# Performance work log

Hardware: AMD Instinct MI355X
Metric: run time of the kernel (lower is better)

The kernel has to match this reference:

```python
import jax, jax.numpy as jnp
import numpy as np

P = 2048
D = 1024
H = 16
DH = D // H
HID = 32


def setup_inputs() -> dict:
    key = jax.random.key(0)
    ks = jax.random.split(key, 10)
    s = 0.02
    return {
        "x": jax.random.normal(ks[0], (P, D), jnp.float32),
        "rel": jax.random.normal(ks[1], (P, P, 2), jnp.float32),
        "w_qkv": jax.random.normal(ks[2], (D, 3 * D), jnp.float32) * s,
        "w_proj": jax.random.normal(ks[3], (D, D), jnp.float32) * s,
        "rpb_w1": jax.random.normal(ks[4], (2, HID), jnp.float32) * s,
        "rpb_b1": jnp.zeros((HID,), jnp.float32),
        "rpb_w2": jax.random.normal(ks[5], (HID, HID), jnp.float32) * s,
        "rpb_b2": jnp.zeros((HID,), jnp.float32),
        "rpb_w3": jax.random.normal(ks[6], (HID, 1), jnp.float32) * s,
        "rpb_b3": jnp.zeros((1,), jnp.float32),
    }


def reference(x, rel, w_qkv, w_proj, rpb_w1, rpb_b1, rpb_w2, rpb_b2, rpb_w3, rpb_b3):
    scale = 1.0 / np.sqrt(DH)
    qkv = x @ w_qkv                                   # [P, 3D]
    q, k, v = jnp.split(qkv, 3, axis=-1)
    # [P, D] -> [H, P, DH]
    q = q.reshape(P, H, DH).transpose(1, 0, 2)
    k = k.reshape(P, H, DH).transpose(1, 0, 2)
    v = v.reshape(P, H, DH).transpose(1, 0, 2)
    logits = jnp.einsum('hpd,hqd->hpq', q, k) * scale  # [H, P, P]
    # RelPosBias MLP: (dx,dy) -> scalar, applied over [P, P, 2]
    hcur = jax.nn.relu(rel @ rpb_w1 + rpb_b1)
    hcur = jax.nn.relu(hcur @ rpb_w2 + rpb_b2)
    bias = (hcur @ rpb_w3 + rpb_b3)[..., 0]            # [P, P]
    logits = logits + bias[None]
    attn = jax.nn.softmax(logits, axis=-1)
    out = jnp.einsum('hpq,hqd->hpd', attn, v)          # [H, P, DH]
    out = out.transpose(1, 0, 2).reshape(P, D)
    return out @ w_proj
```

## Files before the change

kernel.cpp:

```cpp
#include <hip/hip_runtime.h>
#include <hip/hip_bf16.h>
#include <type_traits>

typedef __attribute__((ext_vector_type(8))) short bf16x8;
typedef __attribute__((ext_vector_type(4))) float floatx4;
typedef __attribute__((ext_vector_type(2))) float float2v;

__device__ __forceinline__ float bf2f(unsigned short u) {
    union { unsigned int x; float f; } v; v.x = ((unsigned int)u) << 16; return v.f;
}
__device__ __forceinline__ unsigned short f2bf(float f) {
    union { float f; unsigned int u; } v; v.f = f;
    unsigned int x = v.u;
    unsigned int r = x + 0x7fffu + ((x >> 16) & 1u);
    return (unsigned short)(r >> 16);
}

typedef const __attribute__((address_space(1))) unsigned int u32_g;
typedef __attribute__((address_space(3))) unsigned int u32_l;
__device__ __forceinline__ void gld_lds16(const void* g, void* l) {
    __builtin_amdgcn_global_load_lds((u32_g*)g, (u32_l*)l, 16, 0, 0);
}

__device__ __forceinline__ void trans32(const float* __restrict__ in,
                                        unsigned short* __restrict__ out,
                                        int K, int N, int bx, int by,
                                        unsigned short (*T)[33]) {
    const int n0 = bx * 32, k0 = by * 32;
    const int r = threadIdx.x >> 3;
    const int c4 = (threadIdx.x & 7) * 4;
    float4 v = *reinterpret_cast<const float4*>(in + (size_t)(k0 + r) * N + n0 + c4);
    T[c4 + 0][r] = f2bf(v.x);
    T[c4 + 1][r] = f2bf(v.y);
    T[c4 + 2][r] = f2bf(v.z);
    T[c4 + 3][r] = f2bf(v.w);
    __syncthreads();
    ushort4 o = {T[r][c4], T[r][c4 + 1], T[r][c4 + 2], T[r][c4 + 3]};
    *reinterpret_cast<ushort4*>(out + (size_t)(n0 + r) * K + k0 + c4) = o;
}

__global__ __launch_bounds__(256) void prep(const float* __restrict__ x,
                                            unsigned short* __restrict__ xb,
                                            const float* __restrict__ wq,
                                            unsigned short* __restrict__ wqT,
                                            const float* __restrict__ wp,
                                            unsigned short* __restrict__ wpT) {
    __shared__ unsigned short T[32][33];
    const int b = blockIdx.x;
    if (b < 1024) {
        size_t i = ((size_t)b * 256 + threadIdx.x) * 8;
        float4 a = *reinterpret_cast<const float4*>(x + i);
        float4 c = *reinterpret_cast<const float4*>(x + i + 4);
        unsigned short t[8] = {f2bf(a.x), f2bf(a.y), f2bf(a.z), f2bf(a.w),
                               f2bf(c.x), f2bf(c.y), f2bf(c.z), f2bf(c.w)};
        *reinterpret_cast<uint4*>(xb + i) = *reinterpret_cast<const uint4*>(t);
    } else if (b < 4096) {
        int t = b - 1024;
        trans32(wq, wqT, 1024, 3072, t % 96, t / 96, T);
    } else {
        int t = b - 4096;
        trans32(wp, wpT, 1024, 1024, t % 32, t / 32, T);
    }
}

template<int BN, typename TC>
__global__ __launch_bounds__(256) void gemm_abt(const unsigned short* __restrict__ A,
                                                const unsigned short* __restrict__ Bt,
                                                TC* __restrict__ C,
                                                int M, int N, int K) {
    constexpr int NT = BN / 32;
    __shared__ __align__(16) unsigned short As[64 * 32];
    __shared__ __align__(16) unsigned short Bs[BN * 32];

    const int tid = threadIdx.x;
    const int wave = tid >> 6;
    const int lane = tid & 63;
    const int m15 = lane & 15;
    const int quad = lane >> 4;
    const int wm = wave >> 1;
    const int wn = wave & 1;
    const int m0 = blockIdx.y * 64;
    const int n0 = blockIdx.x * BN;

    const int srow = lane >> 2;
    const int scol = (lane & 3) * 8;

    floatx4 acc[2][NT];
#pragma unroll
    for (int mt = 0; mt < 2; mt++)
#pragma unroll
        for (int nt = 0; nt < NT; nt++) acc[mt][nt] = {0.f, 0.f, 0.f, 0.f};

    for (int k0 = 0; k0 < K; k0 += 32) {
        gld_lds16(A + (size_t)(m0 + wave * 16 + srow) * K + k0 + scol, &As[wave * 16 * 32]);
#pragma unroll
        for (int i = 0; i < BN / 64; i++) {
            int j = wave * (BN / 64) + i;
            gld_lds16(Bt + (size_t)(n0 + j * 16 + srow) * K + k0 + scol, &Bs[j * 16 * 32]);
        }
        __syncthreads();

        bf16x8 a[2];
#pragma unroll
        for (int mt = 0; mt < 2; mt++)
            a[mt] = *reinterpret_cast<bf16x8*>(&As[(wm * 32 + mt * 16 + m15) * 32 + quad * 8]);
#pragma unroll
        for (int nt = 0; nt < NT; nt++) {
            bf16x8 b = *reinterpret_cast<bf16x8*>(&Bs[(wn * (BN / 2) + nt * 16 + m15) * 32 + quad * 8]);
#pragma unroll
            for (int mt = 0; mt < 2; mt++)
                acc[mt][nt] = __builtin_amdgcn_mfma_f32_16x16x32_bf16(a[mt], b, acc[mt][nt], 0, 0, 0);
        }
        __syncthreads();
    }

#pragma unroll
    for (int mt = 0; mt < 2; mt++)
#pragma unroll
        for (int nt = 0; nt < NT; nt++)
#pragma unroll
            for (int i = 0; i < 4; i++) {
                int row = m0 + wm * 32 + mt * 16 + quad * 4 + i;
                int col = n0 + wn * (BN / 2) + nt * 16 + m15;
                if constexpr (std::is_same<TC, float>::value)
                    C[(size_t)row * N + col] = acc[mt][nt][i];
                else
                    C[(size_t)row * N + col] = f2bf(acc[mt][nt][i]);
            }
}

__global__ __launch_bounds__(256) void rpb_mfma_kernel(const float* __restrict__ rel,
                                                       const float* __restrict__ w1,
                                                       const float* __restrict__ b1,
                                                       const float* __restrict__ w2,
                                                       const float* __restrict__ b2,
                                                       const float* __restrict__ w3,
                                                       const float* __restrict__ b3,
                                                       unsigned short* __restrict__ biasb) {
    const int tid = threadIdx.x;
    const int wave = tid >> 6;
    const int lane = tid & 63;
    const int m15 = lane & 15;
    const int quad = lane >> 4;

    bf16x8 af0, af1;
    {
        unsigned short t0[8], t1[8];
#pragma unroll
        for (int j = 0; j < 8; j++) {
            int k = quad * 8 + j;
            t0[j] = f2bf(w2[k * 32 + m15]);
            t1[j] = f2bf(w2[k * 32 + 16 + m15]);
        }
        af0 = *reinterpret_cast<bf16x8*>(t0);
        af1 = *reinterpret_cast<bf16x8*>(t1);
    }

    float2v w1a2[4], w1b2[4], b12[4];
#pragma unroll
    for (int p = 0; p < 4; p++) {
        int base = quad * 8 + 2 * p;
        w1a2[p] = {w1[base], w1[base + 1]};
        w1b2[p] = {w1[32 + base], w1[32 + base + 1]};
        b12[p]  = {b1[base], b1[base + 1]};
    }

    floatx4 b2r0, b2r1;
    float2v w3p00, w3p01, w3p10, w3p11;
    const float LOG2E = 1.44269504f;
    {
        float4 t0 = *reinterpret_cast<const float4*>(b2 + quad * 4);
        float4 t1 = *reinterpret_cast<const float4*>(b2 + 16 + quad * 4);
        b2r0 = {t0.x, t0.y, t0.z, t0.w};
        b2r1 = {t1.x, t1.y, t1.z, t1.w};
        float4 u0 = *reinterpret_cast<const float4*>(w3 + quad * 4);
        float4 u1 = *reinterpret_cast<const float4*>(w3 + 16 + quad * 4);
        w3p00 = {u0.x * LOG2E, u0.y * LOG2E};
        w3p01 = {u0.z * LOG2E, u0.w * LOG2E};
        w3p10 = {u1.x * LOG2E, u1.y * LOG2E};
        w3p11 = {u1.z * LOG2E, u1.w * LOG2E};
    }
    const float b3s = b3[0] * LOG2E;
    const float2v z2 = {0.f, 0.f};

    const int base = blockIdx.x * 1024 + wave * 64;

    for (int it = 0; it < 4; ++it) {
        const int pix0 = base + it * 256;
#pragma unroll
        for (int t = 0; t < 4; t++) {
            const int px = pix0 + t * 16;
            float2 dxy = *reinterpret_cast<const float2*>(rel + (size_t)(px + m15) * 2);
            float2v dx2 = {dxy.x, dxy.x}, dy2 = {dxy.y, dxy.y};

            unsigned int hp[4];
#pragma unroll
            for (int p = 0; p < 4; p++) {
                float2v h = __builtin_elementwise_fma(dx2, w1a2[p],
                             __builtin_elementwise_fma(dy2, w1b2[p], b12[p]));
                h = __builtin_elementwise_max(h, z2);
                hp[p] = __builtin_amdgcn_perm(__float_as_uint(h.y), __float_as_uint(h.x), 0x07060302u);
            }
            bf16x8 hb = *reinterpret_cast<bf16x8*>(hp);

            floatx4 d0 = __builtin_amdgcn_mfma_f32_16x16x32_bf16(af0, hb, b2r0, 0, 0, 0);
            floatx4 d1 = __builtin_amdgcn_mfma_f32_16x16x32_bf16(af1, hb, b2r1, 0, 0, 0);

            float2v m00 = __builtin_elementwise_max(__builtin_shufflevector(d0, d0, 0, 1), z2);
            float2v m01 = __builtin_elementwise_max(__builtin_shufflevector(d0, d0, 2, 3), z2);
            float2v m10 = __builtin_elementwise_max(__builtin_shufflevector(d1, d1, 0, 1), z2);
            float2v m11 = __builtin_elementwise_max(__builtin_shufflevector(d1, d1, 2, 3), z2);
            float2v acc2 = m00 * w3p00;
            acc2 = __builtin_elementwise_fma(m01, w3p01, acc2);
            acc2 = __builtin_elementwise_fma(m10, w3p10, acc2);
            acc2 = __builtin_elementwise_fma(m11, w3p11, acc2);
            float s = acc2.x + acc2.y;

            s += __shfl_xor(s, 16);
            s += __shfl_xor(s, 32);
            s += b3s;

            if (quad == t)
                biasb[(size_t)px + m15] = f2bf(s);
        }
    }
}

__global__ __launch_bounds__(512, 4) void attn_kernel(const unsigned short* __restrict__ qkv,
                                                      const unsigned short* __restrict__ biasb,
                                                      unsigned short* __restrict__ attn_out) {
    const int h = blockIdx.x;
    const int q0 = blockIdx.y * 64;
    __shared__ __align__(16) unsigned short Kst[2][64 * 72];
    __shared__ __align__(16) unsigned short Vst[2][64 * 72];
    __shared__ __align__(16) unsigned short Ps[8][16 * 72];

    const int tid = threadIdx.x;
    const int g = tid >> 8;
    const int w = (tid >> 6) & 3;
    const int lane = tid & 63;
    const int ltid = tid & 255;
    const int m15 = lane & 15;
    const int quad = lane >> 4;

    bf16x8 qf[2];
#pragma unroll
    for (int kh = 0; kh < 2; kh++)
        qf[kh] = *reinterpret_cast<const bf16x8*>(
            qkv + (size_t)(q0 + w * 16 + m15) * 3072 + h * 64 + kh * 32 + quad * 8);

    const int kr0 = ltid >> 3, kd0 = (ltid & 7) * 8;
    const int ka = (ltid & 31) * 2;
    const int vd0 = (ltid >> 5) * 8;

    unsigned short* Kc = Kst[g];
    unsigned short* Vc = Vst[g];
    const size_t kofs = (size_t)g * 1024;

    uint4 kreg0 = *reinterpret_cast<const uint4*>(qkv + (kofs + kr0) * 3072 + 1024 + h * 64 + kd0);
    uint4 kreg1 = *reinterpret_cast<const uint4*>(qkv + (kofs + kr0 + 32) * 3072 + 1024 + h * 64 + kd0);
    uint4 vrega = *reinterpret_cast<const uint4*>(qkv + (kofs + ka) * 3072 + 2048 + h * 64 + vd0);
    uint4 vregb = *reinterpret_cast<const uint4*>(qkv + (kofs + ka + 1) * 3072 + 2048 + h * 64 + vd0);
    unsigned short br[16];
#pragma unroll
    for (int nt = 0; nt < 4; nt++)
#pragma unroll
        for (int i = 0; i < 4; i++)
            br[nt * 4 + i] = biasb[(size_t)(q0 + w * 16 + quad * 4 + i) * 2048 + kofs + nt * 16 + m15];

    float rs[4] = {0.f, 0.f, 0.f, 0.f};
    floatx4 acc[4];
#pragma unroll
    for (int i = 0; i < 4; i++) acc[i] = {0.f, 0.f, 0.f, 0.f};
    const float c1 = 0.125f * 1.44269504f;

    for (int kt = 0; kt < 16; ++kt) {
        __syncthreads();

        *reinterpret_cast<uint4*>(&Kc[kr0 * 72 + kd0]) = kreg0;
        *reinterpret_cast<uint4*>(&Kc[(kr0 + 32) * 72 + kd0]) = kreg1;
        {
            const unsigned int* aw = reinterpret_cast<const unsigned int*>(&vrega);
            const unsigned int* bw = reinterpret_cast<const unsigned int*>(&vregb);
#pragma unroll
            for (int wd = 0; wd < 4; wd++) {
                unsigned int lo = __builtin_amdgcn_perm(bw[wd], aw[wd], 0x05040100u);
                unsigned int hi = __builtin_amdgcn_perm(bw[wd], aw[wd], 0x07060302u);
                *reinterpret_cast<unsigned int*>(&Vc[(vd0 + 2 * wd) * 72 + ka]) = lo;
                *reinterpret_cast<unsigned int*>(&Vc[(vd0 + 2 * wd + 1) * 72 + ka]) = hi;
            }
        }
        __syncthreads();

        if (kt < 15) {
            const size_t kb = kofs + (size_t)(kt + 1) * 64;
            kreg0 = *reinterpret_cast<const uint4*>(qkv + (kb + kr0) * 3072 + 1024 + h * 64 + kd0);
            kreg1 = *reinterpret_cast<const uint4*>(qkv + (kb + kr0 + 32) * 3072 + 1024 + h * 64 + kd0);
            vrega = *reinterpret_cast<const uint4*>(qkv + (kb + ka) * 3072 + 2048 + h * 64 + vd0);
            vregb = *reinterpret_cast<const uint4*>(qkv + (kb + ka + 1) * 3072 + 2048 + h * 64 + vd0);
        }

        floatx4 s[4];
#pragma unroll
        for (int nt = 0; nt < 4; nt++) s[nt] = {0.f, 0.f, 0.f, 0.f};
#pragma unroll
        for (int kh = 0; kh < 2; kh++) {
#pragma unroll
            for (int nt = 0; nt < 4; nt++) {
                bf16x8 b = *reinterpret_cast<bf16x8*>(&Kc[(nt * 16 + m15) * 72 + kh * 32 + quad * 8]);
                s[nt] = __builtin_amdgcn_mfma_f32_16x16x32_bf16(qf[kh], b, s[nt], 0, 0, 0);
            }
        }

        float p[4][4];
#pragma unroll
        for (int nt = 0; nt < 4; nt++)
#pragma unroll
            for (int i = 0; i < 4; i++) {
                float lg = fmaf(s[nt][i], c1, bf2f(br[nt * 4 + i]));
                p[nt][i] = __builtin_amdgcn_exp2f(lg);
                rs[i] += p[nt][i];
            }

        if (kt < 15) {
            const size_t kb = kofs + (size_t)(kt + 1) * 64;
#pragma unroll
            for (int nt = 0; nt < 4; nt++)
#pragma unroll
                for (int i = 0; i < 4; i++)
                    br[nt * 4 + i] = biasb[(size_t)(q0 + w * 16 + quad * 4 + i) * 2048 + kb + nt * 16 + m15];
        }

        unsigned short* Pw = Ps[tid >> 6];
#pragma unroll
        for (int nt = 0; nt < 4; nt++)
#pragma unroll
            for (int i = 0; i < 4; i++)
                Pw[(quad * 4 + i) * 72 + nt * 16 + m15] = f2bf(p[nt][i]);
        __asm__ volatile("s_waitcnt lgkmcnt(0)" ::: "memory");

#pragma unroll
        for (int kh = 0; kh < 2; kh++) {
            bf16x8 a = *reinterpret_cast<bf16x8*>(&Pw[m15 * 72 + kh * 32 + quad * 8]);
#pragma unroll
            for (int nt = 0; nt < 4; nt++) {
                bf16x8 b = *reinterpret_cast<bf16x8*>(&Vc[(nt * 16 + m15) * 72 + kh * 32 + quad * 8]);
                acc[nt] = __builtin_amdgcn_mfma_f32_16x16x32_bf16(a, b, acc[nt], 0, 0, 0);
            }
        }
    }

    float rsum[4];
#pragma unroll
    for (int i = 0; i < 4; i++) {
        float r = rs[i];
        r += __shfl_xor(r, 1);
        r += __shfl_xor(r, 2);
        r += __shfl_xor(r, 4);
        r += __shfl_xor(r, 8);
        rsum[i] = r;
    }

    float* accbuf = reinterpret_cast<float*>(&Kst[0][0]);
    float* lbuf = accbuf + 4096;

    __syncthreads();
    if (g == 1) {
#pragma unroll
        for (int nt = 0; nt < 4; nt++)
#pragma unroll
            for (int i = 0; i < 4; i++)
                accbuf[(w * 16 + quad * 4 + i) * 64 + nt * 16 + m15] = acc[nt][i];
        if (m15 == 0) {
#pragma unroll
            for (int i = 0; i < 4; i++) lbuf[w * 16 + quad * 4 + i] = rsum[i];
        }
    }
    __syncthreads();
    if (g == 0) {
        float linv[4];
#pragma unroll
        for (int i = 0; i < 4; i++)
            linv[i] = 1.f / (rsum[i] + lbuf[w * 16 + quad * 4 + i]);
#pragma unroll
        for (int nt = 0; nt < 4; nt++)
#pragma unroll
            for (int i = 0; i < 4; i++) {
                float o = (acc[nt][i] + accbuf[(w * 16 + quad * 4 + i) * 64 + nt * 16 + m15]) * linv[i];
                int row = q0 + w * 16 + quad * 4 + i;
                int col = h * 64 + nt * 16 + m15;
                attn_out[(size_t)row * 1024 + col] = f2bf(o);
            }
    }
}

extern "C" void kernel_launch(void* const* d_in, const int* in_sizes, int n_in,
                              void* d_out, int out_size, void* d_ws, size_t ws_size,
                              hipStream_t stream) {
    const float* x      = (const float*)d_in[0];
    const float* rel    = (const float*)d_in[1];
    const float* w_qkv  = (const float*)d_in[2];
    const float* w_proj = (const float*)d_in[3];
    const float* w1     = (const float*)d_in[4];
    const float* b1     = (const float*)d_in[5];
    const float* w2     = (const float*)d_in[6];
    const float* b2     = (const float*)d_in[7];
    const float* w3     = (const float*)d_in[8];
    const float* b3     = (const float*)d_in[9];

    char* ws = (char*)d_ws;
    unsigned short* qkv   = (unsigned short*)ws;
    unsigned short* biasb = (unsigned short*)(ws + 12582912);
    unsigned short* xb    = (unsigned short*)(ws + 20971520);
    unsigned short* attn  = xb;
    unsigned short* wqT   = (unsigned short*)(ws + 25165824);
    unsigned short* wpT   = (unsigned short*)(ws + 31457280);
    float* out = (float*)d_out;

    prep<<<5120, 256, 0, stream>>>(x, xb, w_qkv, wqT, w_proj, wpT);
    gemm_abt<128, unsigned short><<<dim3(24, 32), 256, 0, stream>>>(xb, wqT, qkv, 2048, 3072, 1024);
    rpb_mfma_kernel<<<4096, 256, 0, stream>>>(rel, w1, b1, w2, b2, w3, b3, biasb);
    attn_kernel<<<dim3(16, 32), 512, 0, stream>>>(qkv, biasb, attn);
    gemm_abt<64, float><<<dim3(16, 32), 256, 0, stream>>>(attn, wpT, out, 2048, 1024, 1024);
}
```

Measured before the change: 230.6 us.

## Permute bias layout for vectorized loads and add 128x128 QKV GEMM

The RPB kernel now writes bias values in a per-64-column permuted order, so each lane in the attention kernel can fetch its four bias values with one ushort4 load instead of four scalar loads. Separately, the QKV projection moves to a new 128x128-tile GEMM that loads directly into LDS, raising per-block data reuse and halving the number of blocks. The risks are lower occupancy and a single-buffered K loop in the new GEMM. The bias permutation also relies on pix0 and t lining up with the attention kernel's indexing.

```diff
diff --git a/kernel.cpp b/kernel.cpp
--- a/kernel.cpp
+++ b/kernel.cpp
@@ -63,6 +63,67 @@
     }
 }
 
+__global__ __launch_bounds__(256) void gemm128(const unsigned short* __restrict__ A,
+                                               const unsigned short* __restrict__ Bt,
+                                               unsigned short* __restrict__ C,
+                                               int M, int N, int K) {
+    __shared__ __align__(16) unsigned short As[128 * 32];
+    __shared__ __align__(16) unsigned short Bs[128 * 32];
+
+    const int tid = threadIdx.x;
+    const int wave = tid >> 6;
+    const int lane = tid & 63;
+    const int m15 = lane & 15;
+    const int quad = lane >> 4;
+    const int wm = wave >> 1;
+    const int wn = wave & 1;
+    const int m0 = blockIdx.y * 128;
+    const int n0 = blockIdx.x * 128;
+
+    const int srow = lane >> 2;
+    const int scol = (lane & 3) * 8;
+
+    floatx4 acc[4][4];
+#pragma unroll
+    for (int mt = 0; mt < 4; mt++)
+#pragma unroll
+        for (int nt = 0; nt < 4; nt++) acc[mt][nt] = {0.f, 0.f, 0.f, 0.f};
+
+    for (int k0 = 0; k0 < K; k0 += 32) {
+#pragma unroll
+        for (int i = 0; i < 2; i++) {
+            int j = wave * 2 + i;
+            gld_lds16(A + (size_t)(m0 + j * 16 + srow) * K + k0 + scol, &As[j * 16 * 32]);
+            gld_lds16(Bt + (size_t)(n0 + j * 16 + srow) * K + k0 + scol, &Bs[j * 16 * 32]);
+        }
+        __syncthreads();
+
+        bf16x8 a[4];
+#pragma unroll
+        for (int mt = 0; mt < 4; mt++)
+            a[mt] = *reinterpret_cast<bf16x8*>(&As[(wm * 64 + mt * 16 + m15) * 32 + quad * 8]);
+#pragma unroll
+        for (int nt = 0; nt < 4; nt++) {
+            bf16x8 b = *reinterpret_cast<bf16x8*>(&Bs[(wn * 64 + nt * 16 + m15) * 32 + quad * 8]);
+#pragma unroll
+            for (int mt = 0; mt < 4; mt++)
+                acc[mt][nt] = __builtin_amdgcn_mfma_f32_16x16x32_bf16(a[mt], b, acc[mt][nt], 0, 0, 0);
+        }
+        __syncthreads();
+    }
+
+#pragma unroll
+    for (int mt = 0; mt < 4; mt++)
+#pragma unroll
+        for (int nt = 0; nt < 4; nt++)
+#pragma unroll
+            for (int i = 0; i < 4; i++) {
+                int row = m0 + wm * 64 + mt * 16 + quad * 4 + i;
+                int col = n0 + wn * 64 + nt * 16 + m15;
+                C[(size_t)row * N + col] = f2bf(acc[mt][nt][i]);
+            }
+}
+
 template<int BN, typename TC>
 __global__ __launch_bounds__(256) void gemm_abt(const unsigned short* __restrict__ A,
                                                 const unsigned short* __restrict__ Bt,
@@ -221,7 +282,7 @@
             s += b3s;
 
             if (quad == t)
-                biasb[(size_t)px + m15] = f2bf(s);
+                biasb[(size_t)pix0 + m15 * 4 + t] = f2bf(s);
         }
     }
 }
@@ -261,12 +322,14 @@
     uint4 kreg1 = *reinterpret_cast<const uint4*>(qkv + (kofs + kr0 + 32) * 3072 + 1024 + h * 64 + kd0);
     uint4 vrega = *reinterpret_cast<const uint4*>(qkv + (kofs + ka) * 3072 + 2048 + h * 64 + vd0);
     uint4 vregb = *reinterpret_cast<const uint4*>(qkv + (kofs + ka + 1) * 3072 + 2048 + h * 64 + vd0);
+
     unsigned short br[16];
 #pragma unroll
-    for (int nt = 0; nt < 4; nt++)
-#pragma unroll
-        for (int i = 0; i < 4; i++)
-            br[nt * 4 + i] = biasb[(size_t)(q0 + w * 16 + quad * 4 + i) * 2048 + kofs + nt * 16 + m15];
+    for (int i = 0; i < 4; i++) {
+        ushort4 t = *reinterpret_cast<const ushort4*>(
+            biasb + (size_t)(q0 + w * 16 + quad * 4 + i) * 2048 + kofs + m15 * 4);
+        br[0 * 4 + i] = t.x; br[1 * 4 + i] = t.y; br[2 * 4 + i] = t.z; br[3 * 4 + i] = t.w;
+    }
 
     float rs[4] = {0.f, 0.f, 0.f, 0.f};
     floatx4 acc[4];
@@ -325,10 +388,11 @@
         if (kt < 15) {
             const size_t kb = kofs + (size_t)(kt + 1) * 64;
 #pragma unroll
-            for (int nt = 0; nt < 4; nt++)
-#pragma unroll
-                for (int i = 0; i < 4; i++)
-                    br[nt * 4 + i] = biasb[(size_t)(q0 + w * 16 + quad * 4 + i) * 2048 + kb + nt * 16 + m15];
+            for (int i = 0; i < 4; i++) {
+                ushort4 t = *reinterpret_cast<const ushort4*>(
+                    biasb + (size_t)(q0 + w * 16 + quad * 4 + i) * 2048 + kb + m15 * 4);
+                br[0 * 4 + i] = t.x; br[1 * 4 + i] = t.y; br[2 * 4 + i] = t.z; br[3 * 4 + i] = t.w;
+            }
         }
 
         unsigned short* Pw = Ps[tid >> 6];
@@ -418,7 +482,7 @@
     float* out = (float*)d_out;
 
     prep<<<5120, 256, 0, stream>>>(x, xb, w_qkv, wqT, w_proj, wpT);
-    gemm_abt<128, unsigned short><<<dim3(24, 32), 256, 0, stream>>>(xb, wqT, qkv, 2048, 3072, 1024);
+    gemm128<<<dim3(24, 16), 256, 0, stream>>>(xb, wqT, qkv, 2048, 3072, 1024);
     rpb_mfma_kernel<<<4096, 256, 0, stream>>>(rel, w1, b1, w2, b2, w3, b3, biasb);
     attn_kernel<<<dim3(16, 32), 512, 0, stream>>>(qkv, biasb, attn);
     gemm_abt<64, float><<<dim3(16, 32), 256, 0, stream>>>(attn, wpT, out, 2048, 1024, 1024);
```

Result: no change. 232.0 us (+0.6%).
